# Optimization experiments

Measured on AMD Instinct MI355X. Metric: run time of the kernel, lower is better.

Reference implementation:

```python
import jax, jax.numpy as jnp
import numpy as np

B, C, H, W = 128, 768, 14, 14
D = 128          # d_graph
K = 8            # top_k
LN_EPS = 1e-5
NORM_EPS = 1e-12


def setup_inputs() -> dict:
    key = jax.random.key(0)
    ks = jax.random.split(key, 12)
    s = lambda k, shape, fan: jax.random.normal(k, shape, jnp.float32) / np.sqrt(fan)
    return {
        "feat_map": jax.random.normal(ks[0], (B, C, H, W), jnp.float32),
        # node_proj: Linear(C, D) + LayerNorm(D)
        "W_node": s(ks[1], (C, D), C), "b_node": jnp.zeros((D,), jnp.float32),
        "ln_g": jnp.ones((D,), jnp.float32), "ln_b": jnp.zeros((D,), jnp.float32),
        # pos_mlp: Linear(2, 64) -> GELU -> Linear(64, D)
        "Wp1": s(ks[2], (2, 64), 2), "bp1": jnp.zeros((64,), jnp.float32),
        "Wp2": s(ks[3], (64, D), 64), "bp2": jnp.zeros((D,), jnp.float32),
        # edge_mlp: Linear(3D, D) -> GELU -> Linear(D, D)
        "We1": s(ks[4], (3 * D, D), 3 * D), "be1": jnp.zeros((D,), jnp.float32),
        "We2": s(ks[5], (D, D), D), "be2": jnp.zeros((D,), jnp.float32),
    }


def _layernorm(x, g, b):
    mu = jnp.mean(x, axis=-1, keepdims=True)
    var = jnp.mean(jnp.square(x - mu), axis=-1, keepdims=True)
    return (x - mu) * jax.lax.rsqrt(var + LN_EPS) * g + b


def reference(feat_map, W_node, b_node, ln_g, ln_b, Wp1, bp1, Wp2, bp2, We1, be1, We2, be2):
    Bm, Cm, Hm, Wm = feat_map.shape
    N = Hm * Wm
    tokens = feat_map.reshape(Bm, Cm, N).transpose(0, 2, 1)            # [B,N,C]
    nodes = jax.nn.gelu(_layernorm(tokens @ W_node + b_node, ln_g, ln_b), approximate=False)  # [B,N,D]

    ys = jnp.linspace(0.0, 1.0, Hm)
    xs = jnp.linspace(0.0, 1.0, Wm)
    gy, gx = jnp.meshgrid(ys, xs, indexing='ij')
    coords = jnp.stack([gy.reshape(-1), gx.reshape(-1)], axis=-1)       # [N,2]
    coords = jnp.broadcast_to(coords[None], (Bm, N, 2))

    nrm = nodes / jnp.maximum(jnp.linalg.norm(nodes, axis=-1, keepdims=True), NORM_EPS)
    sim = jnp.einsum('bnd,bmd->bnm', nrm, nrm)
    sim = sim - jnp.eye(N, dtype=sim.dtype)[None] * 1e9
    _, adj = jax.lax.top_k(sim, K)                                      # [B,N,K]

    adj_flat = adj.reshape(Bm, N * K, 1)
    neighbor_nodes = jnp.take_along_axis(nodes, adj_flat, axis=1).reshape(Bm, N, K, -1)
    neighbor_coords = jnp.take_along_axis(coords, adj_flat, axis=1).reshape(Bm, N, K, 2)

    disp = neighbor_coords - coords[:, :, None, :]                      # [B,N,K,2]
    spatial_feat = jax.nn.gelu(disp @ Wp1 + bp1, approximate=False) @ Wp2 + bp2  # [B,N,K,D]

    source = jnp.broadcast_to(nodes[:, :, None, :], neighbor_nodes.shape)
    edge_input = jnp.concatenate([source, neighbor_nodes, spatial_feat], axis=-1)  # [B,N,K,3D]
    edges = jax.nn.gelu(edge_input @ We1 + be1, approximate=False) @ We2 + be2
    return nodes, edges, adj
```

## Files before the change

kernel.cpp:

```cpp
#include <hip/hip_runtime.h>

#define BB 128
#define CC 768
#define NN 196
#define DD 128
#define KTOP 8
#define MROWS 25088

typedef unsigned short u16;
typedef unsigned int u32;

__device__ __forceinline__ u16 f2bfu(float x) {
    u32 i; __builtin_memcpy(&i, &x, 4);
    u32 r = (i + 0x7fffu + ((i >> 16) & 1u)) >> 16;
    return (u16)r;
}
__device__ __forceinline__ void unpack2(u32 u, float& f0, float& f1) {
    u32 lo = u << 16, hi = u & 0xffff0000u;
    __builtin_memcpy(&f0, &lo, 4); __builtin_memcpy(&f1, &hi, 4);
}
__device__ __forceinline__ void unpack8(uint4 u, float* f) {
    unpack2(u.x, f[0], f[1]); unpack2(u.y, f[2], f[3]);
    unpack2(u.z, f[4], f[5]); unpack2(u.w, f[6], f[7]);
}
__device__ __forceinline__ float gelu_f(float x) {
    return 0.5f * x * (1.0f + erff(x * 0.70710678118654752f));
}

__global__ __launch_bounds__(256)
void gemm_node_kernel(const float* __restrict__ feat, const float* __restrict__ Wn,
                      float* __restrict__ part)
{
    __shared__ float As[32][64];
    __shared__ float Bs[32][DD];
    const int tid = threadIdx.x;
    const int m0  = blockIdx.x * 64;
    const int k0  = blockIdx.y * 384;

    const int r_ld   = tid & 63;
    const int cl_ld  = tid >> 6;
    const int m_ld   = m0 + r_ld;
    const int b_ld   = m_ld / NN;
    const int n_ld   = m_ld % NN;
    const float* fbase = feat + (size_t)b_ld * CC * NN + n_ld;

    const int rg = tid >> 5;
    const int cg = tid & 31;

    float acc[8][4];
#pragma unroll
    for (int i = 0; i < 8; ++i)
#pragma unroll
        for (int j = 0; j < 4; ++j) acc[i][j] = 0.0f;

    for (int kt = 0; kt < 12; ++kt) {
        const int kbase = k0 + kt * 32;
#pragma unroll
        for (int p = 0; p < 8; ++p) {
            const int cl = cl_ld + 4 * p;
            As[cl][r_ld] = fbase[(size_t)(kbase + cl) * NN];
        }
#pragma unroll
        for (int p = 0; p < 4; ++p) {
            const int q = tid + 256 * p;
            const int cl = q >> 5, d4 = (q & 31) * 4;
            *(float4*)(&Bs[cl][d4]) = *(const float4*)(&Wn[(size_t)(kbase + cl) * DD + d4]);
        }
        __syncthreads();
#pragma unroll
        for (int kk = 0; kk < 32; ++kk) {
            const float4 a0 = *(const float4*)(&As[kk][rg * 8]);
            const float4 a1 = *(const float4*)(&As[kk][rg * 8 + 4]);
            const float4 bv = *(const float4*)(&Bs[kk][cg * 4]);
            const float af[8] = {a0.x, a0.y, a0.z, a0.w, a1.x, a1.y, a1.z, a1.w};
#pragma unroll
            for (int i = 0; i < 8; ++i) {
                acc[i][0] += af[i] * bv.x; acc[i][1] += af[i] * bv.y;
                acc[i][2] += af[i] * bv.z; acc[i][3] += af[i] * bv.w;
            }
        }
        __syncthreads();
    }
    float* op = part + ((size_t)blockIdx.y * MROWS + m0 + rg * 8) * DD + cg * 4;
#pragma unroll
    for (int i = 0; i < 8; ++i) {
        *(float4*)(op + (size_t)i * DD) =
            make_float4(acc[i][0], acc[i][1], acc[i][2], acc[i][3]);
    }
}

__global__ __launch_bounds__(128)
void ln_kernel(const float* __restrict__ part, const float* __restrict__ bnode,
               const float* __restrict__ lng, const float* __restrict__ lnb,
               float* __restrict__ nodes, float* __restrict__ inv_norm)
{
    __shared__ float vals[8][DD];
    __shared__ float stats[8][2];
    const int tid = threadIdx.x;
    const int row0 = blockIdx.x * 8;
    const int d = tid;
    const float bb = bnode[d];
#pragma unroll
    for (int r = 0; r < 8; ++r) {
        const size_t m = row0 + r;
        vals[r][d] = part[m * DD + d] + part[(size_t)(MROWS + m) * DD + d] + bb;
    }
    __syncthreads();
    const int lane = tid & 63, wv = tid >> 6;
    for (int r = wv * 4; r < wv * 4 + 4; ++r) {
        float a0 = vals[r][lane], a1 = vals[r][lane + 64];
        float s = a0 + a1;
#pragma unroll
        for (int off = 32; off > 0; off >>= 1) s += __shfl_xor(s, off);
        const float mu = s * (1.0f / 128.0f);
        float d0 = a0 - mu, d1 = a1 - mu;
        float s2 = d0 * d0 + d1 * d1;
#pragma unroll
        for (int off = 32; off > 0; off >>= 1) s2 += __shfl_xor(s2, off);
        if (lane == 0) { stats[r][0] = mu; stats[r][1] = rsqrtf(s2 * (1.0f/128.0f) + 1e-5f); }
    }
    __syncthreads();
    const float g  = lng[d];
    const float be = lnb[d];
    float acc[8];
#pragma unroll
    for (int r = 0; r < 8; ++r) {
        const float y = (vals[r][d] - stats[r][0]) * stats[r][1] * g + be;
        acc[r] = gelu_f(y);
    }
    __syncthreads();
#pragma unroll
    for (int r = 0; r < 8; ++r) vals[r][d] = acc[r] * acc[r];
#pragma unroll
    for (int r = 0; r < 8; ++r) nodes[(size_t)(row0 + r) * DD + d] = acc[r];
    __syncthreads();
    for (int r = wv * 4; r < wv * 4 + 4; ++r) {
        float s = vals[r][lane] + vals[r][lane + 64];
#pragma unroll
        for (int off = 32; off > 0; off >>= 1) s += __shfl_xor(s, off);
        if (lane == 0) inv_norm[row0 + r] = 1.0f / fmaxf(sqrtf(s), 1e-12f);
    }
}

__global__ __launch_bounds__(256)
void s1n1_kernel(const float* __restrict__ nodes, const float* __restrict__ We1,
                 float* __restrict__ S1, float* __restrict__ N1)
{
    __shared__ float atile[64][DD];
    const int tid = threadIdx.x;
    const int row0 = blockIdx.x * 64;
#pragma unroll
    for (int p = 0; p < 8; ++p) {
        const int idx = tid + 256 * p;
        const int r = idx >> 5, q = idx & 31;
        *(float4*)(&atile[r][q * 4]) = *(const float4*)(&nodes[(size_t)(row0 + r) * DD + q * 4]);
    }
    __syncthreads();
    const int rg = tid >> 5;
    const int cg = tid & 31;
    const int r0 = rg * 8;
    const int c0 = cg * 8;
    const float* wbase = (c0 < DD) ? (We1 + c0) : (We1 + 128 * DD + (c0 - DD));
    float acc[8][8];
#pragma unroll
    for (int i = 0; i < 8; ++i)
#pragma unroll
        for (int j = 0; j < 8; ++j) acc[i][j] = 0.0f;
    for (int k = 0; k < DD; k += 4) {
        float4 av[8];
#pragma unroll
        for (int ri = 0; ri < 8; ++ri) av[ri] = *(const float4*)(&atile[r0 + ri][k]);
#pragma unroll
        for (int kk = 0; kk < 4; ++kk) {
            const float4 w0 = *(const float4*)(wbase + (size_t)(k + kk) * DD);
            const float4 w1 = *(const float4*)(wbase + (size_t)(k + kk) * DD + 4);
            const float wf[8] = {w0.x, w0.y, w0.z, w0.w, w1.x, w1.y, w1.z, w1.w};
#pragma unroll
            for (int ri = 0; ri < 8; ++ri) {
                const float a = (kk == 0) ? av[ri].x : (kk == 1) ? av[ri].y : (kk == 2) ? av[ri].z : av[ri].w;
#pragma unroll
                for (int ci = 0; ci < 8; ++ci) acc[ri][ci] += a * wf[ci];
            }
        }
    }
    float* outp = (c0 < DD) ? (S1 + (size_t)row0 * DD + c0)
                            : (N1 + (size_t)row0 * DD + (c0 - DD));
#pragma unroll
    for (int ri = 0; ri < 8; ++ri) {
        *(float4*)(outp + (size_t)(r0 + ri) * DD) =
            make_float4(acc[ri][0], acc[ri][1], acc[ri][2], acc[ri][3]);
        *(float4*)(outp + (size_t)(r0 + ri) * DD + 4) =
            make_float4(acc[ri][4], acc[ri][5], acc[ri][6], acc[ri][7]);
    }
}

__global__ __launch_bounds__(256)
void sim_kernel(const float* __restrict__ nodes, const float* __restrict__ inv_norm,
                float* __restrict__ sim)
{
    __shared__ float as[28][36];
    __shared__ float bs[NN][36];
    __shared__ float invs[NN];
    const int tid = threadIdx.x;
    const int b  = blockIdx.x / 7;
    const int n0 = (blockIdx.x % 7) * 28;
    const float* nb = nodes + (size_t)b * NN * DD;
    if (tid < NN) invs[tid] = inv_norm[b * NN + tid];
    const bool act = tid < 196;
    const int ai = act ? tid / 28 : 0;
    const int bi = act ? tid % 28 : 0;
    float acc[4][7];
#pragma unroll
    for (int r = 0; r < 4; ++r)
#pragma unroll
        for (int j = 0; j < 7; ++j) acc[r][j] = 0.0f;
    for (int dc = 0; dc < DD; dc += 32) {
        __syncthreads();
        if (tid < 224) {
            const int i = tid >> 3, q = tid & 7;
            *(float4*)(&as[i][q * 4]) = *(const float4*)(&nb[(size_t)(n0 + i) * DD + dc + q * 4]);
        }
        for (int idx = tid; idx < 1568; idx += 256) {
            const int r = idx >> 3, q = idx & 7;
            *(float4*)(&bs[r][q * 4]) = *(const float4*)(&nb[(size_t)r * DD + dc + q * 4]);
        }
        __syncthreads();
        if (act) {
            for (int dd = 0; dd < 32; dd += 4) {
                float4 a4[4], b4[7];
#pragma unroll
                for (int r = 0; r < 4; ++r) a4[r] = *(const float4*)(&as[ai * 4 + r][dd]);
#pragma unroll
                for (int j = 0; j < 7; ++j) b4[j] = *(const float4*)(&bs[bi * 7 + j][dd]);
#pragma unroll
                for (int r = 0; r < 4; ++r)
#pragma unroll
                    for (int j = 0; j < 7; ++j)
                        acc[r][j] += a4[r].x * b4[j].x + a4[r].y * b4[j].y
                                   + a4[r].z * b4[j].z + a4[r].w * b4[j].w;
            }
        }
    }
    if (act) {
#pragma unroll
        for (int r = 0; r < 4; ++r) {
            const int n = n0 + ai * 4 + r;
            const float sn = invs[n];
#pragma unroll
            for (int j = 0; j < 7; ++j) {
                const int m = bi * 7 + j;
                sim[((size_t)b * NN + n) * NN + m] = acc[r][j] * sn * invs[m];
            }
        }
    }
}

__global__ __launch_bounds__(64)
void topk_kernel(const float* __restrict__ sim, int* __restrict__ adj_i,
                 float* __restrict__ adj_o)
{
    const int bn = blockIdx.x;
    const int n = bn % NN;
    const int lane = threadIdx.x;
    const float* srow = sim + (size_t)bn * NN;
    float v[4]; int mi[4];
#pragma unroll
    for (int s = 0; s < 4; ++s) {
        const int m = lane + 64 * s;
        mi[s] = m;
        v[s] = (m < NN && m != n) ? srow[m] : -3.0e38f;
    }
    for (int r = 0; r < KTOP; ++r) {
        float bv = v[0]; int bm = mi[0];
#pragma unroll
        for (int s = 1; s < 4; ++s) { if (v[s] > bv) { bv = v[s]; bm = mi[s]; } }
#pragma unroll
        for (int off = 32; off > 0; off >>= 1) {
            const float ov = __shfl_xor(bv, off);
            const int   om = __shfl_xor(bm, off);
            if (ov > bv || (ov == bv && om < bm)) { bv = ov; bm = om; }
        }
        if (lane == 0) {
            adj_i[bn * KTOP + r] = bm;
            adj_o[bn * KTOP + r] = (float)bm;
        }
#pragma unroll
        for (int s = 0; s < 4; ++s) if (mi[s] == bm) v[s] = -3.0e38f;
    }
}

__global__ __launch_bounds__(128)
void pos_kernel(const float* __restrict__ Wp1, const float* __restrict__ bp1,
                const float* __restrict__ Wp2, const float* __restrict__ bp2,
                const float* __restrict__ We1, float* __restrict__ PC)
{
    __shared__ float t1[64];
    __shared__ float sp[DD];
    const int e = blockIdx.x;
    const int dy = e / 27 - 13, dx = e % 27 - 13;
    const float fy = (float)dy / 13.0f, fx = (float)dx / 13.0f;
    const int tid = threadIdx.x;
    if (tid < 64) {
        const float h = fy * Wp1[tid] + fx * Wp1[64 + tid] + bp1[tid];
        t1[tid] = gelu_f(h);
    }
    __syncthreads();
    float s = bp2[tid];
    for (int j = 0; j < 64; ++j) s += t1[j] * Wp2[j * DD + tid];
    sp[tid] = s;
    __syncthreads();
    float o = 0.0f;
    for (int c = 0; c < DD; ++c) o += sp[c] * We1[(size_t)(256 + c) * DD + tid];
    PC[e * DD + tid] = o;
}

__global__ __launch_bounds__(256)
void edge_kernel(const float* __restrict__ S1, const float* __restrict__ N1,
                 const float* __restrict__ PC, const int* __restrict__ adj_i,
                 const float* __restrict__ be1, const float* __restrict__ We2,
                 const float* __restrict__ be2, float* __restrict__ edges_o)
{
    __shared__ u16 ubf[64][136];
    __shared__ u16 w2[DD][136];
    __shared__ int m_l[64], dx_l[64];
    const int tid = threadIdx.x;
    const int b  = blockIdx.x / 25;
    const int n0 = (blockIdx.x % 25) * 8;
#pragma unroll
    for (int p = 0; p < 16; ++p) {
        const int idx = tid + 256 * p;
        const int r = idx >> 5, c4 = (idx & 31) * 4;
        const float4 w = *(const float4*)(&We2[(size_t)r * DD + c4]);
        ushort4 pk;
        pk.x = f2bfu(w.x); pk.y = f2bfu(w.y); pk.z = f2bfu(w.z); pk.w = f2bfu(w.w);
        *(ushort4*)(&w2[r][c4]) = pk;
    }
    if (tid < 64) {
        const int nl = tid >> 3, k = tid & 7;
        const int n = n0 + nl;
        int mm = 0, di = 0;
        if (n < NN) {
            mm = adj_i[((size_t)b * NN + n) * KTOP + k];
            const int iy = n / 14, ix = n % 14;
            const int my = mm / 14, mx = mm % 14;
            di = (my - iy + 13) * 27 + (mx - ix + 13);
        }
        m_l[tid] = mm; dx_l[tid] = di;
    }
    __syncthreads();
#pragma unroll
    for (int p = 0; p < 8; ++p) {
        const int qi = tid + 256 * p;
        const int r  = qi >> 5;
        const int dq = (qi & 31) * 4;
        const int n  = n0 + (r >> 3);
        ushort4 pk;
        if (n < NN) {
            const float4 s1 = *(const float4*)(&S1[((size_t)b * NN + n) * DD + dq]);
            const float4 n1 = *(const float4*)(&N1[((size_t)b * NN + m_l[r]) * DD + dq]);
            const float4 pc = *(const float4*)(&PC[(size_t)dx_l[r] * DD + dq]);
            pk.x = f2bfu(gelu_f(s1.x + n1.x + pc.x + be1[dq + 0]));
            pk.y = f2bfu(gelu_f(s1.y + n1.y + pc.y + be1[dq + 1]));
            pk.z = f2bfu(gelu_f(s1.z + n1.z + pc.z + be1[dq + 2]));
            pk.w = f2bfu(gelu_f(s1.w + n1.w + pc.w + be1[dq + 3]));
        } else { pk.x = 0; pk.y = 0; pk.z = 0; pk.w = 0; }
        *(ushort4*)(&ubf[r][dq]) = pk;
    }
    __syncthreads();
    const int rg = tid >> 4, cg = tid & 15;
    const int c0 = cg * 8;
    float acc[4][8];
#pragma unroll
    for (int i = 0; i < 4; ++i)
#pragma unroll
        for (int j = 0; j < 8; ++j) acc[i][j] = 0.0f;
    for (int c = 0; c < DD; c += 8) {
        float wf[8][8];
#pragma unroll
        for (int cc = 0; cc < 8; ++cc) {
            const uint4 wu = *(const uint4*)(&w2[c + cc][c0]);
            unpack8(wu, wf[cc]);
        }
#pragma unroll
        for (int ri = 0; ri < 4; ++ri) {
            const int r = rg + 16 * ri;
            const uint4 uu = *(const uint4*)(&ubf[r][c]);
            float uf[8]; unpack8(uu, uf);
#pragma unroll
            for (int cc = 0; cc < 8; ++cc)
#pragma unroll
                for (int ci = 0; ci < 8; ++ci) acc[ri][ci] += uf[cc] * wf[cc][ci];
        }
    }
    float be2f[8];
#pragma unroll
    for (int ci = 0; ci < 8; ++ci) be2f[ci] = be2[c0 + ci];
#pragma unroll
    for (int ri = 0; ri < 4; ++ri) {
        const int r = rg + 16 * ri;
        const int nl = r >> 3, k = r & 7;
        const int n = n0 + nl;
        if (n < NN) {
            float* op = edges_o + (((size_t)b * NN + n) * KTOP + k) * DD + c0;
            *(float4*)(op)     = make_float4(acc[ri][0] + be2f[0], acc[ri][1] + be2f[1],
                                             acc[ri][2] + be2f[2], acc[ri][3] + be2f[3]);
            *(float4*)(op + 4) = make_float4(acc[ri][4] + be2f[4], acc[ri][5] + be2f[5],
                                             acc[ri][6] + be2f[6], acc[ri][7] + be2f[7]);
        }
    }
}

extern "C" void kernel_launch(void* const* d_in, const int* in_sizes, int n_in,
                              void* d_out, int out_size, void* d_ws, size_t ws_size,
                              hipStream_t stream)
{
    const float* feat = (const float*)d_in[0];
    const float* Wn   = (const float*)d_in[1];
    const float* bn   = (const float*)d_in[2];
    const float* lng  = (const float*)d_in[3];
    const float* lnb  = (const float*)d_in[4];
    const float* Wp1  = (const float*)d_in[5];
    const float* bp1  = (const float*)d_in[6];
    const float* Wp2  = (const float*)d_in[7];
    const float* bp2  = (const float*)d_in[8];
    const float* We1  = (const float*)d_in[9];
    const float* be1  = (const float*)d_in[10];
    const float* We2  = (const float*)d_in[11];
    const float* be2  = (const float*)d_in[12];

    float* ws = (float*)d_ws;
    float* part     = ws;
    float* sim      = ws;
    float* S1       = ws + 4917248;
    float* N1       = ws + 8128512;
    float* PC       = ws + 11339776;
    float* inv_norm = ws + 11433088;
    int*   adj_i    = (int*)(ws + 11458176);

    float* out      = (float*)d_out;
    float* nodes    = out;
    float* edges_o  = out + 3211264;
    float* adj_o    = out + 3211264 + 25690112;

    gemm_node_kernel<<<dim3(392, 2), 256, 0, stream>>>(feat, Wn, part);
    ln_kernel<<<3136, 128, 0, stream>>>(part, bn, lng, lnb, nodes, inv_norm);
    s1n1_kernel<<<392, 256, 0, stream>>>(nodes, We1, S1, N1);
    pos_kernel<<<729, 128, 0, stream>>>(Wp1, bp1, Wp2, bp2, We1, PC);
    sim_kernel<<<BB * 7, 256, 0, stream>>>(nodes, inv_norm, sim);
    topk_kernel<<<BB * NN, 64, 0, stream>>>(sim, adj_i, adj_o);
    edge_kernel<<<BB * 25, 256, 0, stream>>>(S1, N1, PC, adj_i, be1, We2, be2, edges_o);
}
```

Baseline: 489.6 us.

## Use bf16 MFMA in edge kernel with We2 prepacked in fragment layout

The second edge-MLP GEMM now runs on `mfma_f32_16x16x32_bf16` instead of scalar FP32 FMAs over unpacked bf16. Each lane builds its A fragment in registers straight from the gathered S1/N1/PC rows, so the A tile no longer goes through LDS. We2 is converted to bf16 once, in MFMA B-fragment order, by 32 extra blocks added to the topk launch and stored in a reused workspace slot. Each edge block then just copies 32KB into LDS rather than reading and converting the full FP32 weight matrix. Output stores become scalar per-lane writes in 16-float runs instead of float4 writes, which may reduce store efficiency.

```diff
diff --git a/kernel.cpp b/kernel.cpp
--- a/kernel.cpp
+++ b/kernel.cpp
@@ -10,18 +10,13 @@
 typedef unsigned short u16;
 typedef unsigned int u32;
 
+typedef __attribute__((ext_vector_type(8))) short bf16x8;
+typedef __attribute__((ext_vector_type(4))) float f32x4;
+
 __device__ __forceinline__ u16 f2bfu(float x) {
     u32 i; __builtin_memcpy(&i, &x, 4);
     u32 r = (i + 0x7fffu + ((i >> 16) & 1u)) >> 16;
     return (u16)r;
-}
-__device__ __forceinline__ void unpack2(u32 u, float& f0, float& f1) {
-    u32 lo = u << 16, hi = u & 0xffff0000u;
-    __builtin_memcpy(&f0, &lo, 4); __builtin_memcpy(&f1, &hi, 4);
-}
-__device__ __forceinline__ void unpack8(uint4 u, float* f) {
-    unpack2(u.x, f[0], f[1]); unpack2(u.y, f[2], f[3]);
-    unpack2(u.z, f[4], f[5]); unpack2(u.w, f[6], f[7]);
 }
 __device__ __forceinline__ float gelu_f(float x) {
     return 0.5f * x * (1.0f + erff(x * 0.70710678118654752f));
@@ -257,9 +252,28 @@
 
 __global__ __launch_bounds__(64)
 void topk_kernel(const float* __restrict__ sim, int* __restrict__ adj_i,
-                 float* __restrict__ adj_o)
+                 float* __restrict__ adj_o, const float* __restrict__ We2,
+                 uint4* __restrict__ W2P)
 {
     const int bn = blockIdx.x;
+    if (bn >= BB * NN) {
+        const int e  = (bn - BB * NN) * 64 + threadIdx.x;
+        const int l  = e & 63;
+        const int fi = e >> 6;
+        const int ks = fi >> 3, ct = fi & 7;
+        const int k0 = ks * 32 + (l >> 4) * 8;
+        const int c  = ct * 16 + (l & 15);
+        u16 v[8];
+#pragma unroll
+        for (int j = 0; j < 8; ++j) v[j] = f2bfu(We2[(size_t)(k0 + j) * DD + c]);
+        uint4 pk;
+        pk.x = (u32)v[0] | ((u32)v[1] << 16);
+        pk.y = (u32)v[2] | ((u32)v[3] << 16);
+        pk.z = (u32)v[4] | ((u32)v[5] << 16);
+        pk.w = (u32)v[6] | ((u32)v[7] << 16);
+        W2P[e] = pk;
+        return;
+    }
     const int n = bn % NN;
     const int lane = threadIdx.x;
     const float* srow = sim + (size_t)bn * NN;
@@ -317,95 +331,88 @@
 __global__ __launch_bounds__(256)
 void edge_kernel(const float* __restrict__ S1, const float* __restrict__ N1,
                  const float* __restrict__ PC, const int* __restrict__ adj_i,
-                 const float* __restrict__ be1, const float* __restrict__ We2,
+                 const float* __restrict__ be1, const uint4* __restrict__ W2P,
                  const float* __restrict__ be2, float* __restrict__ edges_o)
 {
-    __shared__ u16 ubf[64][136];
-    __shared__ u16 w2[DD][136];
-    __shared__ int m_l[64], dx_l[64];
+    __shared__ uint4 ldsB[2048];
     const int tid = threadIdx.x;
     const int b  = blockIdx.x / 25;
     const int n0 = (blockIdx.x % 25) * 8;
-#pragma unroll
-    for (int p = 0; p < 16; ++p) {
-        const int idx = tid + 256 * p;
-        const int r = idx >> 5, c4 = (idx & 31) * 4;
-        const float4 w = *(const float4*)(&We2[(size_t)r * DD + c4]);
-        ushort4 pk;
-        pk.x = f2bfu(w.x); pk.y = f2bfu(w.y); pk.z = f2bfu(w.z); pk.w = f2bfu(w.w);
-        *(ushort4*)(&w2[r][c4]) = pk;
-    }
-    if (tid < 64) {
-        const int nl = tid >> 3, k = tid & 7;
-        const int n = n0 + nl;
-        int mm = 0, di = 0;
+
+#pragma unroll
+    for (int p = 0; p < 8; ++p)
+        ldsB[tid + 256 * p] = W2P[tid + 256 * p];
+
+    const int l  = tid & 63;
+    const int wv = tid >> 6;
+    const int g  = l >> 4;
+    const int rA = wv * 16 + (l & 15);
+    const int nA0 = n0 + (rA >> 3);
+    const int nA  = (nA0 < NN) ? nA0 : 0;
+    const int kA  = rA & 7;
+    const int m   = adj_i[((size_t)b * NN + nA) * KTOP + kA];
+    const int iy = nA / 14, ix = nA % 14;
+    const int my = m / 14,  mx = m % 14;
+    const int di = (my - iy + 13) * 27 + (mx - ix + 13);
+
+    const float* s1r = S1 + ((size_t)b * NN + nA) * DD;
+    const float* n1r = N1 + ((size_t)b * NN + m) * DD;
+    const float* pcr = PC + (size_t)di * DD;
+
+    bf16x8 afr[4];
+#pragma unroll
+    for (int ks = 0; ks < 4; ++ks) {
+        const int k0 = ks * 32 + g * 8;
+        float u[8];
+#pragma unroll
+        for (int h = 0; h < 2; ++h) {
+            const int k = k0 + h * 4;
+            const float4 s1 = *(const float4*)(s1r + k);
+            const float4 n1 = *(const float4*)(n1r + k);
+            const float4 pc = *(const float4*)(pcr + k);
+            const float4 b1 = *(const float4*)(be1 + k);
+            u[h * 4 + 0] = gelu_f(s1.x + n1.x + pc.x + b1.x);
+            u[h * 4 + 1] = gelu_f(s1.y + n1.y + pc.y + b1.y);
+            u[h * 4 + 2] = gelu_f(s1.z + n1.z + pc.z + b1.z);
+            u[h * 4 + 3] = gelu_f(s1.w + n1.w + pc.w + b1.w);
+        }
+        bf16x8 a;
+#pragma unroll
+        for (int j = 0; j < 8; ++j) a[j] = (short)f2bfu(u[j]);
+        afr[ks] = a;
+    }
+    __syncthreads();
+
+    f32x4 acc[8];
+#pragma unroll
+    for (int ct = 0; ct < 8; ++ct) {
+        f32x4 z = {0.0f, 0.0f, 0.0f, 0.0f};
+        acc[ct] = z;
+    }
+#pragma unroll
+    for (int ks = 0; ks < 4; ++ks) {
+#pragma unroll
+        for (int ct = 0; ct < 8; ++ct) {
+            const uint4 bw = ldsB[(ks * 8 + ct) * 64 + l];
+            bf16x8 bf; __builtin_memcpy(&bf, &bw, 16);
+            acc[ct] = __builtin_amdgcn_mfma_f32_16x16x32_bf16(afr[ks], bf, acc[ct], 0, 0, 0);
+        }
+    }
+
+    const int cl  = l & 15;
+    const int rq0 = (l >> 4) * 4;
+    float be2f[8];
+#pragma unroll
+    for (int ct = 0; ct < 8; ++ct) be2f[ct] = be2[ct * 16 + cl];
+#pragma unroll
+    for (int q = 0; q < 4; ++q) {
+        const int r = wv * 16 + rq0 + q;
+        const int n = n0 + (r >> 3);
         if (n < NN) {
-            mm = adj_i[((size_t)b * NN + n) * KTOP + k];
-            const int iy = n / 14, ix = n % 14;
-            const int my = mm / 14, mx = mm % 14;
-            di = (my - iy + 13) * 27 + (mx - ix + 13);
-        }
-        m_l[tid] = mm; dx_l[tid] = di;
-    }
-    __syncthreads();
-#pragma unroll
-    for (int p = 0; p < 8; ++p) {
-        const int qi = tid + 256 * p;
-        const int r  = qi >> 5;
-        const int dq = (qi & 31) * 4;
-        const int n  = n0 + (r >> 3);
-        ushort4 pk;
-        if (n < NN) {
-            const float4 s1 = *(const float4*)(&S1[((size_t)b * NN + n) * DD + dq]);
-            const float4 n1 = *(const float4*)(&N1[((size_t)b * NN + m_l[r]) * DD + dq]);
-            const float4 pc = *(const float4*)(&PC[(size_t)dx_l[r] * DD + dq]);
-            pk.x = f2bfu(gelu_f(s1.x + n1.x + pc.x + be1[dq + 0]));
-            pk.y = f2bfu(gelu_f(s1.y + n1.y + pc.y + be1[dq + 1]));
-            pk.z = f2bfu(gelu_f(s1.z + n1.z + pc.z + be1[dq + 2]));
-            pk.w = f2bfu(gelu_f(s1.w + n1.w + pc.w + be1[dq + 3]));
-        } else { pk.x = 0; pk.y = 0; pk.z = 0; pk.w = 0; }
-        *(ushort4*)(&ubf[r][dq]) = pk;
-    }
-    __syncthreads();
-    const int rg = tid >> 4, cg = tid & 15;
-    const int c0 = cg * 8;
-    float acc[4][8];
-#pragma unroll
-    for (int i = 0; i < 4; ++i)
-#pragma unroll
-        for (int j = 0; j < 8; ++j) acc[i][j] = 0.0f;
-    for (int c = 0; c < DD; c += 8) {
-        float wf[8][8];
-#pragma unroll
-        for (int cc = 0; cc < 8; ++cc) {
-            const uint4 wu = *(const uint4*)(&w2[c + cc][c0]);
-            unpack8(wu, wf[cc]);
-        }
-#pragma unroll
-        for (int ri = 0; ri < 4; ++ri) {
-            const int r = rg + 16 * ri;
-            const uint4 uu = *(const uint4*)(&ubf[r][c]);
-            float uf[8]; unpack8(uu, uf);
-#pragma unroll
-            for (int cc = 0; cc < 8; ++cc)
-#pragma unroll
-                for (int ci = 0; ci < 8; ++ci) acc[ri][ci] += uf[cc] * wf[cc][ci];
-        }
-    }
-    float be2f[8];
-#pragma unroll
-    for (int ci = 0; ci < 8; ++ci) be2f[ci] = be2[c0 + ci];
-#pragma unroll
-    for (int ri = 0; ri < 4; ++ri) {
-        const int r = rg + 16 * ri;
-        const int nl = r >> 3, k = r & 7;
-        const int n = n0 + nl;
-        if (n < NN) {
-            float* op = edges_o + (((size_t)b * NN + n) * KTOP + k) * DD + c0;
-            *(float4*)(op)     = make_float4(acc[ri][0] + be2f[0], acc[ri][1] + be2f[1],
-                                             acc[ri][2] + be2f[2], acc[ri][3] + be2f[3]);
-            *(float4*)(op + 4) = make_float4(acc[ri][4] + be2f[4], acc[ri][5] + be2f[5],
-                                             acc[ri][6] + be2f[6], acc[ri][7] + be2f[7]);
+            float* op = edges_o + (((size_t)b * NN + n) * KTOP + (r & 7)) * DD;
+#pragma unroll
+            for (int ct = 0; ct < 8; ++ct)
+                op[ct * 16 + cl] = acc[ct][q] + be2f[ct];
         }
     }
 }
@@ -436,6 +443,7 @@
     float* PC       = ws + 11339776;
     float* inv_norm = ws + 11433088;
     int*   adj_i    = (int*)(ws + 11458176);
+    uint4* W2P      = (uint4*)(ws + 11433088);
 
     float* out      = (float*)d_out;
     float* nodes    = out;
@@ -447,6 +455,6 @@
     s1n1_kernel<<<392, 256, 0, stream>>>(nodes, We1, S1, N1);
     pos_kernel<<<729, 128, 0, stream>>>(Wp1, bp1, Wp2, bp2, We1, PC);
     sim_kernel<<<BB * 7, 256, 0, stream>>>(nodes, inv_norm, sim);
-    topk_kernel<<<BB * NN, 64, 0, stream>>>(sim, adj_i, adj_o);
-    edge_kernel<<<BB * 25, 256, 0, stream>>>(S1, N1, PC, adj_i, be1, We2, be2, edges_o);
-}
+    topk_kernel<<<BB * NN + 32, 64, 0, stream>>>(sim, adj_i, adj_o, We2, W2P);
+    edge_kernel<<<BB * 25, 256, 0, stream>>>(S1, N1, PC, adj_i, be1, W2P, be2, edges_o);
+}
```

Result: faster. 405.7 us (-17.1%).
